# Kernel optimization log

Measured on AMD Instinct MI355X. Metric: run time of the kernel, lower is better.

Reference implementation:

```python
import jax, jax.numpy as jnp
import numpy as np
from jax import lax

B, TENC, TMEL = 32, 512, 400
E, H, A, P, M, F, K = 512, 512, 512, 256, 128, 32, 31


def setup_inputs() -> dict:
    key = jax.random.key(0)
    ks = jax.random.split(key, 20)
    def rn(i, shape, fan_in):
        return jax.random.normal(ks[i], shape, jnp.float32) / np.float32(np.sqrt(fan_in))
    return dict(
        enc_outputs=jax.random.normal(ks[0], (B, TENC, 2 * E), jnp.float32),
        mel_spec_true=jax.random.normal(ks[1], (B, TMEL, M), jnp.float32),
        text_lens=jax.random.randint(ks[2], (B,), 0, TENC),
        mel_spec_lens=jax.random.randint(ks[3], (B,), 0, TMEL),
        max_text_len=TENC,
        pre_w1=rn(4, (M, P), M), pre_w2=rn(5, (P, P), P),
        attn_wi=rn(6, (P + E, 3 * H), P + E), attn_wh=rn(7, (H, 3 * H), H),
        attn_bi=jnp.zeros((3 * H,), jnp.float32), attn_bh=jnp.zeros((3 * H,), jnp.float32),
        q_w=rn(8, (H, A), H), k_w=rn(9, (2 * E, A), 2 * E),
        score_w=rn(10, (A, 1), A), score_b=jnp.zeros((1,), jnp.float32),
        loc_conv_w=rn(11, (F, 2, K), 2 * K), loc_w=rn(12, (F, A), F), loc_b=jnp.zeros((A,), jnp.float32),
        out_wi=rn(13, (A + H, 3 * H), A + H), out_wh=rn(14, (H, 3 * H), H),
        out_bi=jnp.zeros((3 * H,), jnp.float32), out_bh=jnp.zeros((3 * H,), jnp.float32),
        dec_w=rn(15, (H + A, M), H + A), dec_b=jnp.zeros((M,), jnp.float32),
        gate_w=rn(16, (H + A, 1), H + A), gate_b=jnp.zeros((1,), jnp.float32),
    )


def _gru_step(x, h, wi, wh, bi, bh):
    # single-step torch nn.GRU cell; gate order r, z, n
    gi = x @ wi + bi
    gh = h @ wh + bh
    ir, iz, inn = jnp.split(gi, 3, axis=-1)
    hr, hz, hn = jnp.split(gh, 3, axis=-1)
    r = jax.nn.sigmoid(ir + hr)
    z = jax.nn.sigmoid(iz + hz)
    n = jnp.tanh(inn + r * hn)
    return (1.0 - z) * n + z * h


def reference(enc_outputs, mel_spec_true, text_lens, mel_spec_lens, max_text_len,
              pre_w1, pre_w2, attn_wi, attn_wh, attn_bi, attn_bh,
              q_w, k_w, score_w, score_b, loc_conv_w, loc_w, loc_b,
              out_wi, out_wh, out_bi, out_bh, dec_w, dec_b, gate_w, gate_b):
    Bsz, Tenc, _ = enc_outputs.shape
    Tmel = mel_spec_true.shape[1]
    Hd = attn_wh.shape[0]
    Ad = k_w.shape[1]
    pad = (loc_conv_w.shape[2] - 1) // 2

    keys_p = enc_outputs @ k_w                                # [B,Tenc,A]
    enc_mask = jnp.arange(Tenc)[None, :] > text_lens[:, None]  # True = masked (t > len)

    def prenet(x):  # dropout disabled for determinism
        return jax.nn.relu(jax.nn.relu(x @ pre_w1) @ pre_w2)

    dec_in0 = prenet(jnp.zeros((Bsz, mel_spec_true.shape[2]), enc_outputs.dtype))
    carry0 = (jnp.zeros((Bsz, Hd), jnp.float32), jnp.zeros((Bsz, Hd), jnp.float32),
              jnp.zeros((Bsz, Tenc), jnp.float32), jnp.zeros((Bsz, Tenc), jnp.float32),
              jnp.zeros((Bsz, Ad), jnp.float32), dec_in0)

    def step(carry, _):
        h_attn, h_out, att_w, att_cum, ctx, dec_in = carry
        h_attn = _gru_step(jnp.concatenate([dec_in, ctx], -1), h_attn, attn_wi, attn_wh, attn_bi, attn_bh)
        loc_in = jnp.stack([att_w, att_cum], axis=1)           # [B,2,Tenc]
        loc = lax.conv_general_dilated(loc_in, loc_conv_w, (1,), [(pad, pad)],
                                       dimension_numbers=('NCH', 'OIH', 'NCH'))  # [B,F,Tenc]
        loc = jnp.swapaxes(loc, 1, 2) @ loc_w + loc_b          # [B,Tenc,A]
        q = (h_attn @ q_w)[:, None, :]                         # [B,1,A]
        s = (jnp.tanh(q + keys_p + loc) @ score_w + score_b)[..., 0]  # [B,Tenc]
        s = jnp.where(enc_mask, -jnp.inf, s)
        att_w = jax.nn.softmax(s, axis=1)
        ctx = jnp.einsum('bt,bta->ba', att_w, keys_p)
        att_cum = att_cum + att_w
        h_out = _gru_step(jnp.concatenate([h_attn, ctx], -1), h_out, out_wi, out_wh, out_bi, out_bh)
        att_h = jnp.concatenate([h_out, ctx], -1)
        mel = att_h @ dec_w + dec_b                            # [B,M]
        stop = (att_h @ gate_w + gate_b)[:, 0]                 # [B]
        dec_in = prenet(mel)                                   # teacher_force_ratio = 0
        return (h_attn, h_out, att_w, att_cum, ctx, dec_in), (mel, stop, att_w)

    _, (mels, gates, attns) = lax.scan(step, carry0, None, length=Tmel)
    mels = jnp.swapaxes(mels, 0, 1)    # [B,Tmel,M]
    gates = jnp.swapaxes(gates, 0, 1)  # [B,Tmel]
    attns = jnp.swapaxes(attns, 0, 1)  # [B,Tmel,Tenc]
    mel_mask = jnp.arange(Tmel)[None, :] > mel_spec_lens[:, None]
    masked_mel = jnp.where(mel_mask[:, :, None], 0.0, mels)
    masked_gate = jnp.where(mel_mask, 1000.0, gates)
    return masked_mel, masked_gate, attns, mel_mask
```

## Files before the change

### kernel.cpp

```cpp
#include <hip/hip_runtime.h>
#include <hip/hip_fp16.h>
#include <math.h>

#define NBLK 256
#define NTHR 1024

__device__ __forceinline__ float fast_rcp(float x) {
#if __has_builtin(__builtin_amdgcn_rcpf)
  return __builtin_amdgcn_rcpf(x);
#else
  return 1.f / x;
#endif
}
__device__ __forceinline__ float fast_sigmoid(float x) { return fast_rcp(1.f + __expf(-x)); }
__device__ __forceinline__ float fast_tanh(float x) { return 1.f - 2.f * fast_rcp(1.f + __expf(2.f * x)); }

union HU2 { unsigned int u; __half2 h; };
union HU4 { uint4 u; __half2 h[4]; };
__device__ __forceinline__ float2 cvt2(unsigned int u) { HU2 t; t.u = u; return __half22float2(t.h); }

__device__ __forceinline__ void sta(float* p, float v) {
  __hip_atomic_store(p, v, __ATOMIC_RELAXED, __HIP_MEMORY_SCOPE_AGENT);
}
__device__ __forceinline__ float lda(const float* p) {
  return __hip_atomic_load(p, __ATOMIC_RELAXED, __HIP_MEMORY_SCOPE_AGENT);
}
__device__ __forceinline__ int ldai(const int* p) {
  return __hip_atomic_load(p, __ATOMIC_RELAXED, __HIP_MEMORY_SCOPE_AGENT);
}
__device__ __forceinline__ void ntst(float* p, float v) { __builtin_nontemporal_store(v, p); }

struct Params {
  const float *enc, *pre_w1, *pre_w2, *attn_bi, *attn_bh;
  const float *q_w, *k_w, *score_w, *score_b, *conv_w, *loc_w, *loc_b;
  const float *out_bi, *out_bh, *dec_b, *gate_b;
  const float *attn_wi, *attn_wh, *out_wi, *out_wh, *dec_w, *gate_w;
  const int *text_lens, *mel_lens;
  __half *hkeys, *gw1T, *gw2T, *decT, *pre1T, *pre2T, *gateh, *locwh, *qwT;
  float *hA, *hO, *attw, *attcum, *decin, *ebuf, *zpart, *ctxacc, *ctxacc2, *stateZ;
  float *qbuf;
  int *done, *zdone, *done2, *hAdone, *qdone;
  float *out_mel, *out_gate, *out_attn, *out_mask;
};

__global__ __launch_bounds__(512) void k_keys(Params p) {
  __shared__ float sA[16][132];
  __shared__ float sB[16][68];
  int tid = threadIdx.x;
  int row0 = blockIdx.x * 128, col0 = blockIdx.y * 64;
  float acc[4][4] = {};
  int r = tid >> 2, kq = tid & 3;
  int tx = tid & 15, ty = tid >> 4;
  for (int k0 = 0; k0 < 1024; k0 += 16) {
    __syncthreads();
    float4 a4 = *(const float4*)(p.enc + (size_t)(row0 + r) * 1024 + k0 + kq * 4);
    sA[kq * 4 + 0][r] = a4.x; sA[kq * 4 + 1][r] = a4.y;
    sA[kq * 4 + 2][r] = a4.z; sA[kq * 4 + 3][r] = a4.w;
    if (tid < 256) {
      int kb = tid >> 4, nb = (tid & 15) * 4;
      float4 b4 = *(const float4*)(p.k_w + (size_t)(k0 + kb) * 512 + col0 + nb);
      sB[kb][nb + 0] = b4.x; sB[kb][nb + 1] = b4.y;
      sB[kb][nb + 2] = b4.z; sB[kb][nb + 3] = b4.w;
    }
    __syncthreads();
#pragma unroll
    for (int k = 0; k < 16; k++) {
      float ar[4], br[4];
#pragma unroll
      for (int i = 0; i < 4; i++) { ar[i] = sA[k][ty * 4 + i]; br[i] = sB[k][tx * 4 + i]; }
#pragma unroll
      for (int i = 0; i < 4; i++)
#pragma unroll
        for (int j = 0; j < 4; j++) acc[i][j] = fmaf(ar[i], br[j], acc[i][j]);
    }
  }
#pragma unroll
  for (int i = 0; i < 4; i++)
#pragma unroll
    for (int j = 0; j < 4; j++)
      p.hkeys[(size_t)(row0 + ty * 4 + i) * 512 + col0 + tx * 4 + j] = __float2half(acc[i][j]);
}

__global__ __launch_bounds__(256) void k_repack(Params p) {
  const int gsz = gridDim.x * 256;
  const int t0 = blockIdx.x * 256 + threadIdx.x;
  for (int i = t0; i < 1280 * 512; i += gsz) {
    int r = i >> 9, u = i & 511;
    const float* src = (r < 768) ? p.attn_wi + (size_t)r * 1536 : p.attn_wh + (size_t)(r - 768) * 1536;
    __half2* d = (__half2*)(p.gw1T + ((size_t)i << 2));
    d[0] = __halves2half2(__float2half(src[u]), __float2half(src[512 + u]));
    d[1] = __halves2half2(__float2half(src[1024 + u]), __float2half(0.f));
  }
  for (int i = t0; i < 1536 * 512; i += gsz) {
    int r = i >> 9, u = i & 511;
    const float* src = (r < 1024) ? p.out_wi + (size_t)r * 1536 : p.out_wh + (size_t)(r - 1024) * 1536;
    __half2* d = (__half2*)(p.gw2T + ((size_t)i << 2));
    d[0] = __halves2half2(__float2half(src[u]), __float2half(src[512 + u]));
    d[1] = __halves2half2(__float2half(src[1024 + u]), __float2half(0.f));
  }
  for (int i = t0; i < 512 * 512; i += gsz) {
    int k = i >> 9, a = i & 511;
    p.qwT[(size_t)a * 512 + k] = __float2half(p.q_w[(size_t)k * 512 + a]);
  }
  for (int i = t0; i < 1024 * 128; i += gsz) {
    int k = i >> 7, m = i & 127;
    p.decT[(size_t)m * 1024 + k] = __float2half(p.dec_w[(size_t)k * 128 + m]);
  }
  for (int i = t0; i < 1024; i += gsz) p.gateh[i] = __float2half(p.gate_w[i]);
  for (int i = t0; i < 16384; i += gsz) p.locwh[i] = __float2half(p.loc_w[i]);
  for (int i = t0; i < 128 * 256; i += gsz) {
    int m = i >> 8, pc = i & 255;
    p.pre1T[(size_t)pc * 128 + m] = __float2half(p.pre_w1[(size_t)m * 256 + pc]);
  }
  for (int i = t0; i < 256 * 256; i += gsz) {
    int k = i >> 8, pc = i & 255;
    p.pre2T[(size_t)pc * 256 + k] = __float2half(p.pre_w2[(size_t)k * 256 + pc]);
  }
  for (int i = t0; i < 106496; i += gsz) p.stateZ[i] = 0.f;
  for (int i = t0; i < 16384; i += gsz) p.ctxacc[i] = 0.f;
  for (int i = t0; i < 16384; i += gsz) p.ctxacc2[i] = 0.f;
  for (int i = t0; i < 2048; i += gsz) p.hAdone[i] = 0;
  for (int i = t0; i < 12800; i += gsz) {
    int b = i / 400, t = i - b * 400;
    p.out_mask[i] = (t > p.mel_lens[b]) ? 1.f : 0.f;
  }
}

struct SMemMega {
  __half keysL[64 * 512];
  float ctxL[4][520];
  float hA2[4][520];
  float hO2[4][520];
  float invZ[4];
  union {
    struct { float x[4][264]; float4 part4[16][64]; } gr;
    struct { float locS[64][33]; float aw[94]; float ac[94]; float hA_s[512];
             float qS[512]; float qp2[16][64]; float cpred[8][512]; float eS[64]; } s3;
    struct { float xh[1024]; float red[1024]; float mel[128]; float p1[256]; } s6;
  } u;
};

__device__ __forceinline__ void gchunk(const uint2* __restrict__ w,
                                       const float* __restrict__ x, int ks,
                                       int j0, int j1,
                                       float& a0, float& a1, float& a2) {
#pragma unroll 8
  for (int j = j0; j < j1; ++j) {
    uint2 wv = w[(size_t)j << 13];
    float xv = x[ks + (j << 4)];
    float2 f0 = cvt2(wv.x);
    float nf = cvt2(wv.y).x;
    a0 = fmaf(xv, f0.x, a0);
    a1 = fmaf(xv, f0.y, a1);
    a2 = fmaf(xv, nf, a2);
  }
}

__global__ __launch_bounds__(NTHR) void mega(Params p) {
  __shared__ SMemMega sm;
  const int blk = blockIdx.x, tid = threadIdx.x;
  const int ug = blk & 31, bg = blk >> 5, b0 = bg * 4;
  const int bS = blk & 31, t8 = blk >> 5, t0g = t8 << 6;
  const int bgS = bS >> 2;

  const int u_ = tid & 15, b2_ = (tid >> 4) & 3, ks_ = tid >> 6;
  const int uG_ = (ug << 4) + u_;
  const uint2* w1 = (const uint2*)p.gw1T + ((size_t)ks_ << 9) + uG_;
  const uint2* w2 = (const uint2*)p.gw2T + ((size_t)ks_ << 9) + uG_;

  {
    const uint4* src = (const uint4*)(p.hkeys + (((size_t)(bS << 9) + t0g) << 9));
    uint4* dst = (uint4*)sm.keysL;
    for (int i = tid; i < 4096; i += NTHR) dst[i] = src[i];
    for (int i = tid; i < 2048; i += NTHR) {
      sm.ctxL[i >> 9][i & 511] = 0.f;
      sm.hA2[i >> 9][i & 511] = 0.f;
      sm.hO2[i >> 9][i & 511] = 0.f;
    }
  }
  __syncthreads();

  float g1r = 0.f, g1z = 0.f, g1ni = 0.f, g1nh = 0.f;

#pragma clang loop unroll(disable)
  for (int step = 0; step < 400; step++) {
    const int par = step & 1;
    float* hA_prev = p.hA + par * 16384;
    float* hA_next = p.hA + (par ^ 1) * 16384;
    float* hO_prev = p.hO + par * 16384;
    float* hO_next = p.hO + (par ^ 1) * 16384;
    float* cCur = par ? p.ctxacc2 : p.ctxacc;
    float* cNxt = par ? p.ctxacc : p.ctxacc2;

    float r2 = 0.f, z2 = 0.f, ni2 = 0.f, nh2 = 0.f;

    {
      if (step > 0) {
        if (tid == 0) {
          while (ldai(&p.done2[bg * 16]) < 16 * step)
            __builtin_amdgcn_s_sleep(2);
        }
        __syncthreads();
      }
      for (int i = tid; i < 1024; i += NTHR)
        sm.u.gr.x[i >> 8][i & 255] = lda(&p.decin[((b0 + (i >> 8)) << 8) + (i & 255)]);
      for (int i = tid; i < 2048; i += NTHR)
        sm.hO2[i >> 9][i & 511] = lda(&hO_prev[((b0 + (i >> 9)) << 9) + (i & 511)]);
      __syncthreads();
      gchunk(w1, &sm.u.gr.x[b2_][0], ks_, 0, 16, g1r, g1z, g1ni);
      sm.u.gr.part4[ks_][(u_ << 2) + b2_] = make_float4(g1r, g1z, g1ni, g1nh);
      __syncthreads();
      if (tid < 64) {
        int uu = tid >> 2, bb2 = tid & 3;
        float4 s = make_float4(0.f, 0.f, 0.f, 0.f);
#pragma unroll
        for (int l = 0; l < 16; l++) {
          float4 v = sm.u.gr.part4[l][(uu << 2) + bb2];
          s.x += v.x; s.y += v.y; s.z += v.z; s.w += v.w;
        }
        int uGf = (ug << 4) + uu;
        float r = fast_sigmoid(s.x + p.attn_bi[uGf] + p.attn_bh[uGf]);
        float z = fast_sigmoid(s.y + p.attn_bi[512 + uGf] + p.attn_bh[512 + uGf]);
        float n = fast_tanh(s.z + p.attn_bi[1024 + uGf] + r * (s.w + p.attn_bh[1024 + uGf]));
        float hv = lda(&hA_prev[((b0 + bb2) << 9) + uGf]);
        sta(&hA_next[((b0 + bb2) << 9) + uGf], (1.f - z) * n + z * hv);
      }
      asm volatile("s_waitcnt vmcnt(0)" ::: "memory");
      if (tid == 0) atomicAdd(&p.hAdone[bg * 16], 1);
      gchunk(w2, &sm.hO2[b2_][0] - 1024, ks_, 64, 96, r2, z2, nh2);
    }

    {
      __syncthreads();
      for (int j = tid; j < 94; j += NTHR) {
        int pp = t0g - 15 + j;
        bool ok = (unsigned)pp < 512u;
        sm.u.s3.aw[j] = ok ? lda(&p.attw[(bS << 9) + pp]) : 0.f;
        sm.u.s3.ac[j] = ok ? lda(&p.attcum[(bS << 9) + pp]) : 0.f;
      }
      if (t8 == 0) {
        for (int i = tid; i < 512; i += NTHR) sta(&cNxt[(bS << 9) + i], 0.f);
      }
      __syncthreads();
      const int tlen = p.text_lens[bS];
      for (int i = tid; i < 2048; i += NTHR) {
        int tt = i >> 5, f = i & 31;
        const float* w0 = p.conv_w + f * 62;
        float a = 0.f;
#pragma unroll
        for (int k = 0; k < 31; k++)
          a = fmaf(w0[k], sm.u.s3.aw[tt + k], fmaf(w0[31 + k], sm.u.s3.ac[tt + k], a));
        sm.u.s3.locS[tt][f] = a;
      }
      if (tid == 0) {
        while (ldai(&p.hAdone[bgS * 16]) < 32 * (step + 1))
          __builtin_amdgcn_s_sleep(2);
      }
      __syncthreads();
      if (tid < 512) sm.u.s3.hA_s[tid] = lda(&hA_next[(bS << 9) + tid]);
      __syncthreads();
      {
        int a = tid & 63, ks = tid >> 6;
        const HU4* qp = (const HU4*)(p.qwT + (size_t)(t0g + a) * 512 + ks * 32);
        float q0 = 0.f, q1 = 0.f;
#pragma unroll
        for (int it = 0; it < 4; it++) {
          HU4 raw = qp[it];
          int kb = ks * 32 + it * 8;
#pragma unroll
          for (int h2 = 0; h2 < 4; h2++) {
            float2 w = __half22float2(raw.h[h2]);
            q0 = fmaf(sm.u.s3.hA_s[kb + h2 * 2], w.x, q0);
            q1 = fmaf(sm.u.s3.hA_s[kb + h2 * 2 + 1], w.y, q1);
          }
        }
        sm.u.s3.qp2[ks][a] = q0 + q1;
      }
      __syncthreads();
      if (tid < 64) {
        float s = 0.f;
#pragma unroll
        for (int l = 0; l < 16; l++) s += sm.u.s3.qp2[l][tid];
        sta(&p.qbuf[(bS << 9) + t0g + tid], s + p.loc_b[t0g + tid]);
      }
      if (tid == 0) {
        asm volatile("s_waitcnt vmcnt(0)" ::: "memory");
        atomicAdd(&p.qdone[bS * 16], 1);
      }
      const int lane = tid & 63, wv = tid >> 6;
      float acc[4][8] = {};
#pragma unroll 4
      for (int f = 0; f < 32; f++) {
        HU4 rw; rw.u = *(const uint4*)(p.locwh + (size_t)f * 512 + lane * 8);
        float2 w0 = __half22float2(rw.h[0]), w1 = __half22float2(rw.h[1]);
        float2 w2v = __half22float2(rw.h[2]), w3 = __half22float2(rw.h[3]);
#pragma unroll
        for (int j = 0; j < 4; j++) {
          float lf = sm.u.s3.locS[wv * 4 + j][f];
          acc[j][0] = fmaf(lf, w0.x, acc[j][0]); acc[j][1] = fmaf(lf, w0.y, acc[j][1]);
          acc[j][2] = fmaf(lf, w1.x, acc[j][2]); acc[j][3] = fmaf(lf, w1.y, acc[j][3]);
          acc[j][4] = fmaf(lf, w2v.x, acc[j][4]); acc[j][5] = fmaf(lf, w2v.y, acc[j][5]);
          acc[j][6] = fmaf(lf, w3.x, acc[j][6]); acc[j][7] = fmaf(lf, w3.y, acc[j][7]);
        }
      }
      if (tid == 0) {
        while (ldai(&p.qdone[bS * 16]) < 8 * (step + 1))
          __builtin_amdgcn_s_sleep(2);
      }
      __syncthreads();
      if (tid < 512) sm.u.s3.qS[tid] = lda(&p.qbuf[(bS << 9) + tid]);
      __syncthreads();
      float4 qA = *(const float4*)&sm.u.s3.qS[lane * 8];
      float4 qB = *(const float4*)&sm.u.s3.qS[lane * 8 + 4];
#pragma unroll
      for (int j = 0; j < 4; j++) {
        int tL = wv * 4 + j;
        HU4 raw; raw.u = *(const uint4*)&sm.keysL[tL * 512 + lane * 8];
        float2 k0 = __half22float2(raw.h[0]), k1 = __half22float2(raw.h[1]);
        float2 k2 = __half22float2(raw.h[2]), k3 = __half22float2(raw.h[3]);
        acc[j][0] += qA.x + k0.x; acc[j][1] += qA.y + k0.y;
        acc[j][2] += qA.z + k1.x; acc[j][3] += qA.w + k1.y;
        acc[j][4] += qB.x + k2.x; acc[j][5] += qB.y + k2.y;
        acc[j][6] += qB.z + k3.x; acc[j][7] += qB.w + k3.y;
      }
      float4 sA = *(const float4*)(p.score_w + lane * 8);
      float4 sB = *(const float4*)(p.score_w + lane * 8 + 4);
      float sbias = p.score_b[0];
      float e_reg[4];
#pragma unroll
      for (int j = 0; j < 4; j++) {
        float pv = fast_tanh(acc[j][0]) * sA.x + fast_tanh(acc[j][1]) * sA.y +
                   fast_tanh(acc[j][2]) * sA.z + fast_tanh(acc[j][3]) * sA.w +
                   fast_tanh(acc[j][4]) * sB.x + fast_tanh(acc[j][5]) * sB.y +
                   fast_tanh(acc[j][6]) * sB.z + fast_tanh(acc[j][7]) * sB.w;
#pragma unroll
        for (int off = 32; off > 0; off >>= 1) pv += __shfl_xor(pv, off, 64);
        int t = t0g + wv * 4 + j;
        e_reg[j] = (t > tlen) ? 0.f : __expf(pv + sbias);
      }
      if (lane == 0) {
#pragma unroll
        for (int j = 0; j < 4; j++) sm.u.s3.eS[wv * 4 + j] = e_reg[j];
      }
      float cp[8] = {0.f, 0.f, 0.f, 0.f, 0.f, 0.f, 0.f, 0.f};
#pragma unroll
      for (int j = 0; j < 4; j++) {
        int tL = wv * 4 + j;
        HU4 raw; raw.u = *(const uint4*)&sm.keysL[tL * 512 + lane * 8];
        float2 k0 = __half22float2(raw.h[0]), k1 = __half22float2(raw.h[1]);
        float2 k2 = __half22float2(raw.h[2]), k3 = __half22float2(raw.h[3]);
        float e = e_reg[j];
        cp[0] = fmaf(e, k0.x, cp[0]); cp[1] = fmaf(e, k0.y, cp[1]);
        cp[2] = fmaf(e, k1.x, cp[2]); cp[3] = fmaf(e, k1.y, cp[3]);
        cp[4] = fmaf(e, k2.x, cp[4]); cp[5] = fmaf(e, k2.y, cp[5]);
        cp[6] = fmaf(e, k3.x, cp[6]); cp[7] = fmaf(e, k3.y, cp[7]);
      }
      __syncthreads();
      if (wv < 8) {
        float4* r0 = (float4*)&sm.u.s3.cpred[wv][lane * 8];
        r0[0] = make_float4(cp[0], cp[1], cp[2], cp[3]);
        r0[1] = make_float4(cp[4], cp[5], cp[6], cp[7]);
      }
      __syncthreads();
      if (wv >= 8) {
        float* r0 = &sm.u.s3.cpred[wv - 8][lane * 8];
#pragma unroll
        for (int i = 0; i < 8; i++) r0[i] += cp[i];
      }
      __syncthreads();
      if (tid < 512) {
        float s = 0.f;
#pragma unroll
        for (int j = 0; j < 8; j++) s += sm.u.s3.cpred[j][tid];
        atomicAdd(&cCur[(bS << 9) + tid], s);
      }
      if (tid < 64) {
        float e = sm.u.s3.eS[tid];
        sta(&p.ebuf[(bS << 9) + t0g + tid], e);
        float z = e;
#pragma unroll
        for (int off = 32; off > 0; off >>= 1) z += __shfl_xor(z, off, 64);
        if (tid == 0) sta(&p.zpart[bS * 8 + t8], z);
      }
      if (tid < 512 && (tid & 63) == 0) {
        asm volatile("s_waitcnt vmcnt(0)" ::: "memory");
        atomicAdd(&p.zdone[bgS * 16], 1);
      }
      if (tid == 0) {
        while (ldai(&p.hAdone[bg * 16]) < 32 * (step + 1))
          __builtin_amdgcn_s_sleep(2);
      }
      __syncthreads();
      for (int i = tid; i < 2048; i += NTHR)
        sm.hA2[i >> 9][i & 511] = lda(&hA_next[((b0 + (i >> 9)) << 9) + (i & 511)]);
      __syncthreads();
      gchunk(w2, &sm.hA2[b2_][0], ks_, 0, 32, r2, z2, ni2);
    }

    {
      if (tid == 0) {
        while (ldai(&p.zdone[bg * 16]) < 256 * (step + 1))
          __builtin_amdgcn_s_sleep(2);
      }
      __syncthreads();
      if (tid < 4) {
        float Z = 0.f;
#pragma unroll
        for (int j = 0; j < 8; j++) Z += lda(&p.zpart[(b0 + tid) * 8 + j]);
        sm.invZ[tid] = fast_rcp(Z);
      }
      __syncthreads();
      for (int i = tid; i < 2048; i += NTHR) {
        int b2 = i >> 9, a = i & 511;
        sm.ctxL[b2][a] = lda(&cCur[((b0 + b2) << 9) + a]) * sm.invZ[b2];
      }
      if (ug < 4 && tid < 512) {
        const int bb = b0 + ug;
        float v = lda(&p.ebuf[(bb << 9) + tid]) * sm.invZ[ug];
        sta(&p.attw[(bb << 9) + tid], v);
        float oc = lda(&p.attcum[(bb << 9) + tid]);
        sta(&p.attcum[(bb << 9) + tid], oc + v);
        ntst(&p.out_attn[(size_t)bb * 204800 + (size_t)step * 512 + tid], v);
      }
      __syncthreads();
      gchunk(w2, &sm.ctxL[b2_][0] - 512, ks_, 32, 64, r2, z2, ni2);
      sm.u.gr.part4[ks_][(u_ << 2) + b2_] = make_float4(r2, z2, ni2, nh2);
      __syncthreads();
      if (tid < 64) {
        int uu = tid >> 2, bb2 = tid & 3;
        float4 s = make_float4(0.f, 0.f, 0.f, 0.f);
#pragma unroll
        for (int l = 0; l < 16; l++) {
          float4 v = sm.u.gr.part4[l][(uu << 2) + bb2];
          s.x += v.x; s.y += v.y; s.z += v.z; s.w += v.w;
        }
        int uGf = (ug << 4) + uu;
        float r = fast_sigmoid(s.x + p.out_bi[uGf] + p.out_bh[uGf]);
        float z = fast_sigmoid(s.y + p.out_bi[512 + uGf] + p.out_bh[512 + uGf]);
        float n = fast_tanh(s.z + p.out_bi[1024 + uGf] + r * (s.w + p.out_bh[1024 + uGf]));
        float hv = sm.hO2[bb2][uGf];
        sta(&hO_next[((b0 + bb2) << 9) + uGf], (1.f - z) * n + z * hv);
      }
      asm volatile("s_waitcnt vmcnt(0)" ::: "memory");
      if (tid == 0) atomicAdd(&p.done[bg * 16], 1);
      g1r = 0.f; g1z = 0.f; g1ni = 0.f; g1nh = 0.f;
      if (step < 399) {
        gchunk(w1, &sm.ctxL[b2_][0] - 256, ks_, 16, 48, g1r, g1z, g1ni);
        gchunk(w1, &sm.hA2[b2_][0] - 768, ks_, 48, 80, g1r, g1z, g1nh);
      }
      if (ug < 4) {
        const int bb = b0 + ug;
        if (tid == 0) {
          while (ldai(&p.done[bg * 16]) < 32 * (step + 1))
            __builtin_amdgcn_s_sleep(2);
        }
        __syncthreads();
        sm.u.s6.xh[tid] = (tid < 512) ? lda(&hO_next[(bb << 9) + tid])
                                      : sm.ctxL[ug][tid - 512];
        __syncthreads();
        bool masked = step > p.mel_lens[bb];
        {
          int m = tid & 127, ks = tid >> 7;
          const HU4* dp = (const HU4*)(p.decT + (size_t)m * 1024 + ks * 128);
          float a = 0.f;
#pragma unroll 4
          for (int it = 0; it < 16; it++) {
            HU4 raw = dp[it];
            int kb = ks * 128 + it * 8;
#pragma unroll
            for (int h2 = 0; h2 < 4; h2++) {
              float2 w = __half22float2(raw.h[h2]);
              a = fmaf(sm.u.s6.xh[kb + h2 * 2], w.x, a);
              a = fmaf(sm.u.s6.xh[kb + h2 * 2 + 1], w.y, a);
            }
          }
          sm.u.s6.red[tid] = a;
        }
        __syncthreads();
        if (tid < 128) {
          float mv = p.dec_b[tid];
#pragma unroll
          for (int j = 0; j < 8; j++) mv += sm.u.s6.red[tid + j * 128];
          sm.u.s6.mel[tid] = mv;
          ntst(&p.out_mel[(size_t)bb * 51200 + (size_t)step * 128 + tid], masked ? 0.f : mv);
        }
        __syncthreads();
        sm.u.s6.red[tid] = sm.u.s6.xh[tid] * __half2float(p.gateh[tid]);
        __syncthreads();
        if (tid < 64) {
          float g = 0.f;
#pragma unroll
          for (int j = 0; j < 16; j++) g += sm.u.s6.red[tid + j * 64];
#pragma unroll
          for (int off = 32; off > 0; off >>= 1) g += __shfl_xor(g, off, 64);
          if (tid == 0) ntst(&p.out_gate[bb * 400 + step], masked ? 1000.f : (g + p.gate_b[0]));
        }
        __syncthreads();
        {
          int pc = tid & 255, ks = tid >> 8;
          const HU4* wp = (const HU4*)(p.pre1T + (size_t)pc * 128 + ks * 32);
          float a = 0.f;
#pragma unroll
          for (int it = 0; it < 4; it++) {
            HU4 raw = wp[it];
            int kb = ks * 32 + it * 8;
#pragma unroll
            for (int h2 = 0; h2 < 4; h2++) {
              float2 w = __half22float2(raw.h[h2]);
              a = fmaf(sm.u.s6.mel[kb + h2 * 2], w.x, a);
              a = fmaf(sm.u.s6.mel[kb + h2 * 2 + 1], w.y, a);
            }
          }
          sm.u.s6.red[tid] = a;
        }
        __syncthreads();
        if (tid < 256) {
          float a = sm.u.s6.red[tid] + sm.u.s6.red[tid + 256] +
                    sm.u.s6.red[tid + 512] + sm.u.s6.red[tid + 768];
          sm.u.s6.p1[tid] = fmaxf(a, 0.f);
        }
        __syncthreads();
        {
          int pc = tid & 255, ks = tid >> 8;
          const HU4* wp = (const HU4*)(p.pre2T + (size_t)pc * 256 + ks * 64);
          float a = 0.f;
#pragma unroll
          for (int it = 0; it < 8; it++) {
            HU4 raw = wp[it];
            int kb = ks * 64 + it * 8;
#pragma unroll
            for (int h2 = 0; h2 < 4; h2++) {
              float2 w = __half22float2(raw.h[h2]);
              a = fmaf(sm.u.s6.p1[kb + h2 * 2], w.x, a);
              a = fmaf(sm.u.s6.p1[kb + h2 * 2 + 1], w.y, a);
            }
          }
          sm.u.s6.red[tid] = a;
        }
        __syncthreads();
        if (tid < 256) {
          float a = sm.u.s6.red[tid] + sm.u.s6.red[tid + 256] +
                    sm.u.s6.red[tid + 512] + sm.u.s6.red[tid + 768];
          sta(&p.decin[(bb << 8) + tid], fmaxf(a, 0.f));
        }
        if (tid < 256 && (tid & 63) == 0) {
          asm volatile("s_waitcnt vmcnt(0)" ::: "memory");
          atomicAdd(&p.done2[bg * 16], 1);
        }
      }
    }
  }
}

extern "C" void kernel_launch(void* const* d_in, const int* in_sizes, int n_in,
                              void* d_out, int out_size, void* d_ws, size_t ws_size,
                              hipStream_t stream) {
  Params p;
  p.enc       = (const float*)d_in[0];
  p.text_lens = (const int*)d_in[2];
  p.mel_lens  = (const int*)d_in[3];
  p.pre_w1    = (const float*)d_in[5];
  p.pre_w2    = (const float*)d_in[6];
  p.attn_wi   = (const float*)d_in[7];
  p.attn_wh   = (const float*)d_in[8];
  p.attn_bi   = (const float*)d_in[9];
  p.attn_bh   = (const float*)d_in[10];
  p.q_w       = (const float*)d_in[11];
  p.k_w       = (const float*)d_in[12];
  p.score_w   = (const float*)d_in[13];
  p.score_b   = (const float*)d_in[14];
  p.conv_w    = (const float*)d_in[15];
  p.loc_w     = (const float*)d_in[16];
  p.loc_b     = (const float*)d_in[17];
  p.out_wi    = (const float*)d_in[18];
  p.out_wh    = (const float*)d_in[19];
  p.out_bi    = (const float*)d_in[20];
  p.out_bh    = (const float*)d_in[21];
  p.dec_w     = (const float*)d_in[22];
  p.dec_b     = (const float*)d_in[23];
  p.gate_w    = (const float*)d_in[24];
  p.gate_b    = (const float*)d_in[25];

  float* ws = (float*)d_ws;
  p.hkeys  = (__half*)(ws);
  p.gw1T   = (__half*)(ws + 4194304);
  p.gw2T   = (__half*)(ws + 5505024);
  p.decT   = (__half*)(ws + 7077888);
  p.pre1T  = (__half*)(ws + 7143424);
  p.pre2T  = (__half*)(ws + 7159808);
  p.gateh  = (__half*)(ws + 7192576);
  p.locwh  = (__half*)(ws + 7193088);
  p.qwT    = (__half*)(ws + 7201280);
  p.hA     = ws + 7332352;
  p.hO     = ws + 7365120;
  p.attw   = ws + 7397888;
  p.attcum = ws + 7414272;
  p.decin  = ws + 7430656;
  p.stateZ = p.hA;
  p.ebuf   = ws + 7438848;
  p.zpart  = ws + 7455232;
  p.ctxacc = ws + 7455488;
  p.ctxacc2 = ws + 7472416;
  int* fb  = (int*)(ws + 7488800);
  p.hAdone = fb;
  p.zdone  = fb + 128;
  p.done   = fb + 256;
  p.done2  = fb + 384;
  p.qdone  = fb + 512;
  p.qbuf   = ws + 7490848;
  float* out = (float*)d_out;
  p.out_mel  = out;
  p.out_gate = out + 1638400;
  p.out_attn = out + 1651200;
  p.out_mask = out + 8204800;

  k_repack<<<2048, 256, 0, stream>>>(p);
  k_keys<<<dim3(128, 8), 512, 0, stream>>>(p);
  void* args[] = { (void*)&p };
  hipLaunchCooperativeKernel((const void*)mega, dim3(NBLK), dim3(NTHR), args, 0, stream);
}
```

Before: 37.33 ms.

## Distribute mel/gate projection across GRU blocks via partial sums and offload attention writes

Each block that computes a 16-unit slice of the output GRU state now also computes partial dot products of its hO/ctx slice with dec_w and gate_w (read as fp32). These partials go to a global buffer, which the owning block sums over 32 slices. The per-batch block no longer does the full 1024x128 decoder matvec on the serial critical path. The attention-weight normalisation and stores move from the ug<4 blocks to ug 4..7, so that work runs in parallel. Other changes come with this: a one-time global barrier (melpart reuses the hkeys workspace region), higher done counters, and extra synchronisation and global traffic for the partials.

```diff
diff --git a/kernel.cpp b/kernel.cpp
--- a/kernel.cpp
+++ b/kernel.cpp
@@ -36,10 +36,10 @@
   const float *out_bi, *out_bh, *dec_b, *gate_b;
   const float *attn_wi, *attn_wh, *out_wi, *out_wh, *dec_w, *gate_w;
   const int *text_lens, *mel_lens;
-  __half *hkeys, *gw1T, *gw2T, *decT, *pre1T, *pre2T, *gateh, *locwh, *qwT;
+  __half *hkeys, *gw1T, *gw2T, *pre1T, *pre2T, *locwh, *qwT;
   float *hA, *hO, *attw, *attcum, *decin, *ebuf, *zpart, *ctxacc, *ctxacc2, *stateZ;
-  float *qbuf;
-  int *done, *zdone, *done2, *hAdone, *qdone;
+  float *qbuf, *melpart, *gatepart;
+  int *done, *zdone, *done2, *hAdone, *qdone, *initbar;
   float *out_mel, *out_gate, *out_attn, *out_mask;
 };
 
@@ -102,11 +102,6 @@
     int k = i >> 9, a = i & 511;
     p.qwT[(size_t)a * 512 + k] = __float2half(p.q_w[(size_t)k * 512 + a]);
   }
-  for (int i = t0; i < 1024 * 128; i += gsz) {
-    int k = i >> 7, m = i & 127;
-    p.decT[(size_t)m * 1024 + k] = __float2half(p.dec_w[(size_t)k * 128 + m]);
-  }
-  for (int i = t0; i < 1024; i += gsz) p.gateh[i] = __float2half(p.gate_w[i]);
   for (int i = t0; i < 16384; i += gsz) p.locwh[i] = __float2half(p.loc_w[i]);
   for (int i = t0; i < 128 * 256; i += gsz) {
     int m = i >> 8, pc = i & 255;
@@ -133,10 +128,10 @@
   float hO2[4][520];
   float invZ[4];
   union {
-    struct { float x[4][264]; float4 part4[16][64]; } gr;
+    struct { float x[4][264]; float4 part4[16][64]; float hOslice[4][16]; } gr;
     struct { float locS[64][33]; float aw[94]; float ac[94]; float hA_s[512];
              float qS[512]; float qp2[16][64]; float cpred[8][512]; float eS[64]; } s3;
-    struct { float xh[1024]; float red[1024]; float mel[128]; float p1[256]; } s6;
+    struct { float red[1024]; float mel[132]; float p1[264]; } s6;
   } u;
 };
 
@@ -179,6 +174,11 @@
     }
   }
   __syncthreads();
+  if (tid == 0) {
+    atomicAdd(p.initbar, 1);
+    while (ldai(p.initbar) < NBLK) __builtin_amdgcn_s_sleep(2);
+  }
+  __syncthreads();
 
   float g1r = 0.f, g1z = 0.f, g1ni = 0.f, g1nh = 0.f;
 
@@ -197,7 +197,7 @@
     {
       if (step > 0) {
         if (tid == 0) {
-          while (ldai(&p.done2[bg * 16]) < 16 * step)
+          while (ldai(&p.done2[bg * 16]) < 48 * step)
             __builtin_amdgcn_s_sleep(2);
         }
         __syncthreads();
@@ -414,14 +414,6 @@
         int b2 = i >> 9, a = i & 511;
         sm.ctxL[b2][a] = lda(&cCur[((b0 + b2) << 9) + a]) * sm.invZ[b2];
       }
-      if (ug < 4 && tid < 512) {
-        const int bb = b0 + ug;
-        float v = lda(&p.ebuf[(bb << 9) + tid]) * sm.invZ[ug];
-        sta(&p.attw[(bb << 9) + tid], v);
-        float oc = lda(&p.attcum[(bb << 9) + tid]);
-        sta(&p.attcum[(bb << 9) + tid], oc + v);
-        ntst(&p.out_attn[(size_t)bb * 204800 + (size_t)step * 512 + tid], v);
-      }
       __syncthreads();
       gchunk(w2, &sm.ctxL[b2_][0] - 512, ks_, 32, 64, r2, z2, ni2);
       sm.u.gr.part4[ks_][(u_ << 2) + b2_] = make_float4(r2, z2, ni2, nh2);
@@ -439,10 +431,37 @@
         float z = fast_sigmoid(s.y + p.out_bi[512 + uGf] + p.out_bh[512 + uGf]);
         float n = fast_tanh(s.z + p.out_bi[1024 + uGf] + r * (s.w + p.out_bh[1024 + uGf]));
         float hv = sm.hO2[bb2][uGf];
-        sta(&hO_next[((b0 + bb2) << 9) + uGf], (1.f - z) * n + z * hv);
-      }
-      asm volatile("s_waitcnt vmcnt(0)" ::: "memory");
-      if (tid == 0) atomicAdd(&p.done[bg * 16], 1);
+        float hnew = (1.f - z) * n + z * hv;
+        sta(&hO_next[((b0 + bb2) << 9) + uGf], hnew);
+        sm.u.gr.hOslice[bb2][uu] = hnew;
+      }
+      __syncthreads();
+      if (tid < 512) {
+        int b = tid >> 7, m = tid & 127;
+        const float* dwH = p.dec_w + ((size_t)(ug << 4)) * 128 + m;
+        const float* dwC = p.dec_w + ((size_t)(512 + (ug << 4))) * 128 + m;
+        float a = 0.f;
+#pragma unroll
+        for (int u = 0; u < 16; u++) {
+          a = fmaf(sm.u.gr.hOslice[b][u], dwH[(size_t)u * 128], a);
+          a = fmaf(sm.ctxL[b][(ug << 4) + u], dwC[(size_t)u * 128], a);
+        }
+        sta(&p.melpart[((((b0 + b) << 5) | ug) << 7) + m], a);
+        if (m == 0) {
+          const float* gw = p.gate_w + (ug << 4);
+          float g = 0.f;
+#pragma unroll
+          for (int u = 0; u < 16; u++) {
+            g = fmaf(sm.u.gr.hOslice[b][u], gw[u], g);
+            g = fmaf(sm.ctxL[b][(ug << 4) + u], gw[512 + u], g);
+          }
+          sta(&p.gatepart[((b0 + b) << 5) | ug], g);
+        }
+      }
+      if (tid < 512 && (tid & 63) == 0) {
+        asm volatile("s_waitcnt vmcnt(0)" ::: "memory");
+        atomicAdd(&p.done[bg * 16], 1);
+      }
       g1r = 0.f; g1z = 0.f; g1ni = 0.f; g1nh = 0.f;
       if (step < 399) {
         gchunk(w1, &sm.ctxL[b2_][0] - 256, ks_, 16, 48, g1r, g1z, g1ni);
@@ -451,49 +470,26 @@
       if (ug < 4) {
         const int bb = b0 + ug;
         if (tid == 0) {
-          while (ldai(&p.done[bg * 16]) < 32 * (step + 1))
+          while (ldai(&p.done[bg * 16]) < 256 * (step + 1))
             __builtin_amdgcn_s_sleep(2);
         }
-        __syncthreads();
-        sm.u.s6.xh[tid] = (tid < 512) ? lda(&hO_next[(bb << 9) + tid])
-                                      : sm.ctxL[ug][tid - 512];
         __syncthreads();
         bool masked = step > p.mel_lens[bb];
-        {
-          int m = tid & 127, ks = tid >> 7;
-          const HU4* dp = (const HU4*)(p.decT + (size_t)m * 1024 + ks * 128);
-          float a = 0.f;
-#pragma unroll 4
-          for (int it = 0; it < 16; it++) {
-            HU4 raw = dp[it];
-            int kb = ks * 128 + it * 8;
-#pragma unroll
-            for (int h2 = 0; h2 < 4; h2++) {
-              float2 w = __half22float2(raw.h[h2]);
-              a = fmaf(sm.u.s6.xh[kb + h2 * 2], w.x, a);
-              a = fmaf(sm.u.s6.xh[kb + h2 * 2 + 1], w.y, a);
-            }
-          }
-          sm.u.s6.red[tid] = a;
-        }
-        __syncthreads();
         if (tid < 128) {
+          const float* mp = p.melpart + (((size_t)(bb << 5)) << 7) + tid;
           float mv = p.dec_b[tid];
 #pragma unroll
-          for (int j = 0; j < 8; j++) mv += sm.u.s6.red[tid + j * 128];
+          for (int g = 0; g < 32; g++) mv += lda(mp + (g << 7));
           sm.u.s6.mel[tid] = mv;
           ntst(&p.out_mel[(size_t)bb * 51200 + (size_t)step * 128 + tid], masked ? 0.f : mv);
         }
-        __syncthreads();
-        sm.u.s6.red[tid] = sm.u.s6.xh[tid] * __half2float(p.gateh[tid]);
-        __syncthreads();
-        if (tid < 64) {
-          float g = 0.f;
-#pragma unroll
-          for (int j = 0; j < 16; j++) g += sm.u.s6.red[tid + j * 64];
-#pragma unroll
-          for (int off = 32; off > 0; off >>= 1) g += __shfl_xor(g, off, 64);
-          if (tid == 0) ntst(&p.out_gate[bb * 400 + step], masked ? 1000.f : (g + p.gate_b[0]));
+        if (tid >= 128 && tid < 192) {
+          int l = tid & 63;
+          float g = (l < 32) ? lda(&p.gatepart[(bb << 5) + l]) : 0.f;
+#pragma unroll
+          for (int off = 16; off > 0; off >>= 1) g += __shfl_xor(g, off, 64);
+          if (l == 0)
+            ntst(&p.out_gate[bb * 400 + step], masked ? 1000.f : (g + p.gate_b[0]));
         }
         __syncthreads();
         {
@@ -544,6 +540,19 @@
           sta(&p.decin[(bb << 8) + tid], fmaxf(a, 0.f));
         }
         if (tid < 256 && (tid & 63) == 0) {
+          asm volatile("s_waitcnt vmcnt(0)" ::: "memory");
+          atomicAdd(&p.done2[bg * 16], 1);
+        }
+      } else if (ug < 8) {
+        const int bj = ug - 4, bb = b0 + bj;
+        if (tid < 512) {
+          float v = lda(&p.ebuf[(bb << 9) + tid]) * sm.invZ[bj];
+          sta(&p.attw[(bb << 9) + tid], v);
+          float oc = lda(&p.attcum[(bb << 9) + tid]);
+          sta(&p.attcum[(bb << 9) + tid], oc + v);
+          ntst(&p.out_attn[(size_t)bb * 204800 + (size_t)step * 512 + tid], v);
+        }
+        if (tid < 512 && (tid & 63) == 0) {
           asm volatile("s_waitcnt vmcnt(0)" ::: "memory");
           atomicAdd(&p.done2[bg * 16], 1);
         }
@@ -583,12 +592,12 @@
 
   float* ws = (float*)d_ws;
   p.hkeys  = (__half*)(ws);
+  p.melpart = ws;
+  p.gatepart = ws + 131072;
   p.gw1T   = (__half*)(ws + 4194304);
   p.gw2T   = (__half*)(ws + 5505024);
-  p.decT   = (__half*)(ws + 7077888);
   p.pre1T  = (__half*)(ws + 7143424);
   p.pre2T  = (__half*)(ws + 7159808);
-  p.gateh  = (__half*)(ws + 7192576);
   p.locwh  = (__half*)(ws + 7193088);
   p.qwT    = (__half*)(ws + 7201280);
   p.hA     = ws + 7332352;
@@ -607,6 +616,7 @@
   p.done   = fb + 256;
   p.done2  = fb + 384;
   p.qdone  = fb + 512;
+  p.initbar = fb + 1920;
   p.qbuf   = ws + 7490848;
   float* out = (float*)d_out;
   p.out_mel  = out;
```

New measurement: 46.05 ms. 1.23x slower.

## Replicate decoder/prenet per block to remove the done2 grid barrier

Applied to the files above, without the earlier changes.

Every block in a batch group now recomputes the mel projection and both prenet layers for its 4 batch rows redundantly, keeping decoder input in shared memory instead of waiting on a done2 flag from 4 designated blocks. hA and hO previous values are also read from local shared copies. The attention-weight normalisation and attcum update move to different blocks after the GRU, with a new per-batch adone counter that the attention stage waits on. This swaps a cross-block dependency on the serial critical path for redundant matmul work in every block, and risks ordering or visibility problems in the new flag protocol.

```diff
diff --git a/kernel.cpp b/kernel.cpp
--- a/kernel.cpp
+++ b/kernel.cpp
@@ -39,7 +39,7 @@
   __half *hkeys, *gw1T, *gw2T, *decT, *pre1T, *pre2T, *gateh, *locwh, *qwT;
   float *hA, *hO, *attw, *attcum, *decin, *ebuf, *zpart, *ctxacc, *ctxacc2, *stateZ;
   float *qbuf;
-  int *done, *zdone, *done2, *hAdone, *qdone;
+  int *done, *zdone, *hAdone, *qdone, *adone;
   float *out_mel, *out_gate, *out_attn, *out_mask;
 };
 
@@ -131,12 +131,13 @@
   float ctxL[4][520];
   float hA2[4][520];
   float hO2[4][520];
+  float decinL[4][264];
   float invZ[4];
   union {
-    struct { float x[4][264]; float4 part4[16][64]; } gr;
+    struct { float pad[1056]; float4 part4[16][64]; } gr;
     struct { float locS[64][33]; float aw[94]; float ac[94]; float hA_s[512];
              float qS[512]; float qp2[16][64]; float cpred[8][512]; float eS[64]; } s3;
-    struct { float xh[1024]; float red[1024]; float mel[128]; float p1[256]; } s6;
+    struct { float red[4][264]; float mel[4][132]; float p1[4][264]; } s6;
   } u;
 };
 
@@ -177,6 +178,7 @@
       sm.hA2[i >> 9][i & 511] = 0.f;
       sm.hO2[i >> 9][i & 511] = 0.f;
     }
+    for (int i = tid; i < 1024; i += NTHR) sm.decinL[i >> 8][i & 255] = 0.f;
   }
   __syncthreads();
 
@@ -185,9 +187,7 @@
 #pragma clang loop unroll(disable)
   for (int step = 0; step < 400; step++) {
     const int par = step & 1;
-    float* hA_prev = p.hA + par * 16384;
     float* hA_next = p.hA + (par ^ 1) * 16384;
-    float* hO_prev = p.hO + par * 16384;
     float* hO_next = p.hO + (par ^ 1) * 16384;
     float* cCur = par ? p.ctxacc2 : p.ctxacc;
     float* cNxt = par ? p.ctxacc : p.ctxacc2;
@@ -195,19 +195,7 @@
     float r2 = 0.f, z2 = 0.f, ni2 = 0.f, nh2 = 0.f;
 
     {
-      if (step > 0) {
-        if (tid == 0) {
-          while (ldai(&p.done2[bg * 16]) < 16 * step)
-            __builtin_amdgcn_s_sleep(2);
-        }
-        __syncthreads();
-      }
-      for (int i = tid; i < 1024; i += NTHR)
-        sm.u.gr.x[i >> 8][i & 255] = lda(&p.decin[((b0 + (i >> 8)) << 8) + (i & 255)]);
-      for (int i = tid; i < 2048; i += NTHR)
-        sm.hO2[i >> 9][i & 511] = lda(&hO_prev[((b0 + (i >> 9)) << 9) + (i & 511)]);
-      __syncthreads();
-      gchunk(w1, &sm.u.gr.x[b2_][0], ks_, 0, 16, g1r, g1z, g1ni);
+      gchunk(w1, &sm.decinL[b2_][0], ks_, 0, 16, g1r, g1z, g1ni);
       sm.u.gr.part4[ks_][(u_ << 2) + b2_] = make_float4(g1r, g1z, g1ni, g1nh);
       __syncthreads();
       if (tid < 64) {
@@ -222,7 +210,7 @@
         float r = fast_sigmoid(s.x + p.attn_bi[uGf] + p.attn_bh[uGf]);
         float z = fast_sigmoid(s.y + p.attn_bi[512 + uGf] + p.attn_bh[512 + uGf]);
         float n = fast_tanh(s.z + p.attn_bi[1024 + uGf] + r * (s.w + p.attn_bh[1024 + uGf]));
-        float hv = lda(&hA_prev[((b0 + bb2) << 9) + uGf]);
+        float hv = sm.hA2[bb2][uGf];
         sta(&hA_next[((b0 + bb2) << 9) + uGf], (1.f - z) * n + z * hv);
       }
       asm volatile("s_waitcnt vmcnt(0)" ::: "memory");
@@ -232,6 +220,13 @@
 
     {
       __syncthreads();
+      if (step > 0) {
+        if (tid == 0) {
+          while (ldai(&p.adone[bS * 16]) < 8 * step)
+            __builtin_amdgcn_s_sleep(2);
+        }
+        __syncthreads();
+      }
       for (int j = tid; j < 94; j += NTHR) {
         int pp = t0g - 15 + j;
         bool ok = (unsigned)pp < 512u;
@@ -414,14 +409,6 @@
         int b2 = i >> 9, a = i & 511;
         sm.ctxL[b2][a] = lda(&cCur[((b0 + b2) << 9) + a]) * sm.invZ[b2];
       }
-      if (ug < 4 && tid < 512) {
-        const int bb = b0 + ug;
-        float v = lda(&p.ebuf[(bb << 9) + tid]) * sm.invZ[ug];
-        sta(&p.attw[(bb << 9) + tid], v);
-        float oc = lda(&p.attcum[(bb << 9) + tid]);
-        sta(&p.attcum[(bb << 9) + tid], oc + v);
-        ntst(&p.out_attn[(size_t)bb * 204800 + (size_t)step * 512 + tid], v);
-      }
       __syncthreads();
       gchunk(w2, &sm.ctxL[b2_][0] - 512, ks_, 32, 64, r2, z2, ni2);
       sm.u.gr.part4[ks_][(u_ << 2) + b2_] = make_float4(r2, z2, ni2, nh2);
@@ -443,111 +430,132 @@
       }
       asm volatile("s_waitcnt vmcnt(0)" ::: "memory");
       if (tid == 0) atomicAdd(&p.done[bg * 16], 1);
+      if (ug >= 4 && ug < 8) {
+        const int bj = ug - 4, bb = b0 + bj;
+        if (tid < 512) {
+          float v = lda(&p.ebuf[(bb << 9) + tid]) * sm.invZ[bj];
+          sta(&p.attw[(bb << 9) + tid], v);
+          float oc = lda(&p.attcum[(bb << 9) + tid]);
+          sta(&p.attcum[(bb << 9) + tid], oc + v);
+          ntst(&p.out_attn[(size_t)bb * 204800 + (size_t)step * 512 + tid], v);
+        }
+        if (tid < 512 && (tid & 63) == 0) {
+          asm volatile("s_waitcnt vmcnt(0)" ::: "memory");
+          atomicAdd(&p.adone[bb * 16], 1);
+        }
+      }
       g1r = 0.f; g1z = 0.f; g1ni = 0.f; g1nh = 0.f;
       if (step < 399) {
         gchunk(w1, &sm.ctxL[b2_][0] - 256, ks_, 16, 48, g1r, g1z, g1ni);
         gchunk(w1, &sm.hA2[b2_][0] - 768, ks_, 48, 80, g1r, g1z, g1nh);
       }
-      if (ug < 4) {
-        const int bb = b0 + ug;
-        if (tid == 0) {
-          while (ldai(&p.done[bg * 16]) < 32 * (step + 1))
-            __builtin_amdgcn_s_sleep(2);
-        }
-        __syncthreads();
-        sm.u.s6.xh[tid] = (tid < 512) ? lda(&hO_next[(bb << 9) + tid])
-                                      : sm.ctxL[ug][tid - 512];
-        __syncthreads();
-        bool masked = step > p.mel_lens[bb];
-        {
-          int m = tid & 127, ks = tid >> 7;
-          const HU4* dp = (const HU4*)(p.decT + (size_t)m * 1024 + ks * 128);
-          float a = 0.f;
-#pragma unroll 4
-          for (int it = 0; it < 16; it++) {
-            HU4 raw = dp[it];
-            int kb = ks * 128 + it * 8;
-#pragma unroll
-            for (int h2 = 0; h2 < 4; h2++) {
-              float2 w = __half22float2(raw.h[h2]);
-              a = fmaf(sm.u.s6.xh[kb + h2 * 2], w.x, a);
-              a = fmaf(sm.u.s6.xh[kb + h2 * 2 + 1], w.y, a);
-            }
+      if (tid == 0) {
+        while (ldai(&p.done[bg * 16]) < 32 * (step + 1))
+          __builtin_amdgcn_s_sleep(2);
+      }
+      __syncthreads();
+      for (int i = tid; i < 2048; i += NTHR)
+        sm.hO2[i >> 9][i & 511] = lda(&hO_next[((b0 + (i >> 9)) << 9) + (i & 511)]);
+      __syncthreads();
+      if (tid < 256) {
+        int m = tid & 127, kh = tid >> 7;
+        const HU4* dp = (const HU4*)(p.decT + (size_t)m * 1024 + kh * 512);
+        const float* base = kh ? &sm.ctxL[0][0] : &sm.hO2[0][0];
+        float a0 = 0.f, a1 = 0.f, a2 = 0.f, a3 = 0.f;
+#pragma unroll 8
+        for (int it = 0; it < 64; it++) {
+          HU4 raw = dp[it];
+          int kb = it * 8;
+#pragma unroll
+          for (int h2 = 0; h2 < 4; h2++) {
+            float2 w = __half22float2(raw.h[h2]);
+            int k0 = kb + h2 * 2, k1 = k0 + 1;
+            a0 = fmaf(base[k0], w.x, fmaf(base[k1], w.y, a0));
+            a1 = fmaf(base[520 + k0], w.x, fmaf(base[520 + k1], w.y, a1));
+            a2 = fmaf(base[1040 + k0], w.x, fmaf(base[1040 + k1], w.y, a2));
+            a3 = fmaf(base[1560 + k0], w.x, fmaf(base[1560 + k1], w.y, a3));
           }
-          sm.u.s6.red[tid] = a;
-        }
-        __syncthreads();
-        if (tid < 128) {
-          float mv = p.dec_b[tid];
-#pragma unroll
-          for (int j = 0; j < 8; j++) mv += sm.u.s6.red[tid + j * 128];
-          sm.u.s6.mel[tid] = mv;
-          ntst(&p.out_mel[(size_t)bb * 51200 + (size_t)step * 128 + tid], masked ? 0.f : mv);
-        }
-        __syncthreads();
-        sm.u.s6.red[tid] = sm.u.s6.xh[tid] * __half2float(p.gateh[tid]);
-        __syncthreads();
-        if (tid < 64) {
-          float g = 0.f;
-#pragma unroll
-          for (int j = 0; j < 16; j++) g += sm.u.s6.red[tid + j * 64];
-#pragma unroll
-          for (int off = 32; off > 0; off >>= 1) g += __shfl_xor(g, off, 64);
-          if (tid == 0) ntst(&p.out_gate[bb * 400 + step], masked ? 1000.f : (g + p.gate_b[0]));
-        }
-        __syncthreads();
-        {
-          int pc = tid & 255, ks = tid >> 8;
-          const HU4* wp = (const HU4*)(p.pre1T + (size_t)pc * 128 + ks * 32);
-          float a = 0.f;
-#pragma unroll
-          for (int it = 0; it < 4; it++) {
-            HU4 raw = wp[it];
-            int kb = ks * 32 + it * 8;
-#pragma unroll
-            for (int h2 = 0; h2 < 4; h2++) {
-              float2 w = __half22float2(raw.h[h2]);
-              a = fmaf(sm.u.s6.mel[kb + h2 * 2], w.x, a);
-              a = fmaf(sm.u.s6.mel[kb + h2 * 2 + 1], w.y, a);
-            }
+        }
+        int idx = kh * 128 + m;
+        sm.u.s6.red[0][idx] = a0; sm.u.s6.red[1][idx] = a1;
+        sm.u.s6.red[2][idx] = a2; sm.u.s6.red[3][idx] = a3;
+      }
+      __syncthreads();
+      if (tid < 512) {
+        int b = tid >> 7, m = tid & 127;
+        float mv = p.dec_b[m] + sm.u.s6.red[b][m] + sm.u.s6.red[b][128 + m];
+        sm.u.s6.mel[b][m] = mv;
+        if (ug < 4 && b == ug) {
+          int bb = b0 + b;
+          bool masked = step > p.mel_lens[bb];
+          ntst(&p.out_mel[(size_t)bb * 51200 + (size_t)step * 128 + m], masked ? 0.f : mv);
+        }
+      }
+      __syncthreads();
+      if (ug < 4 && tid >= 512 && tid < 768) {
+        int t = tid - 512;
+        float g = sm.hO2[ug][t] * __half2float(p.gateh[t]) +
+                  sm.hO2[ug][t + 256] * __half2float(p.gateh[t + 256]) +
+                  sm.ctxL[ug][t] * __half2float(p.gateh[512 + t]) +
+                  sm.ctxL[ug][t + 256] * __half2float(p.gateh[768 + t]);
+        sm.u.s6.red[0][t] = g;
+      }
+      if (tid < 256) {
+        int pc = tid;
+        const HU4* wp = (const HU4*)(p.pre1T + (size_t)pc * 128);
+        float a0 = 0.f, a1 = 0.f, a2 = 0.f, a3 = 0.f;
+#pragma unroll
+        for (int it = 0; it < 16; it++) {
+          HU4 raw = wp[it];
+          int kb = it * 8;
+#pragma unroll
+          for (int h2 = 0; h2 < 4; h2++) {
+            float2 w = __half22float2(raw.h[h2]);
+            int k0 = kb + h2 * 2, k1 = k0 + 1;
+            a0 = fmaf(sm.u.s6.mel[0][k0], w.x, fmaf(sm.u.s6.mel[0][k1], w.y, a0));
+            a1 = fmaf(sm.u.s6.mel[1][k0], w.x, fmaf(sm.u.s6.mel[1][k1], w.y, a1));
+            a2 = fmaf(sm.u.s6.mel[2][k0], w.x, fmaf(sm.u.s6.mel[2][k1], w.y, a2));
+            a3 = fmaf(sm.u.s6.mel[3][k0], w.x, fmaf(sm.u.s6.mel[3][k1], w.y, a3));
           }
-          sm.u.s6.red[tid] = a;
-        }
-        __syncthreads();
-        if (tid < 256) {
-          float a = sm.u.s6.red[tid] + sm.u.s6.red[tid + 256] +
-                    sm.u.s6.red[tid + 512] + sm.u.s6.red[tid + 768];
-          sm.u.s6.p1[tid] = fmaxf(a, 0.f);
-        }
-        __syncthreads();
-        {
-          int pc = tid & 255, ks = tid >> 8;
-          const HU4* wp = (const HU4*)(p.pre2T + (size_t)pc * 256 + ks * 64);
-          float a = 0.f;
-#pragma unroll
-          for (int it = 0; it < 8; it++) {
-            HU4 raw = wp[it];
-            int kb = ks * 64 + it * 8;
-#pragma unroll
-            for (int h2 = 0; h2 < 4; h2++) {
-              float2 w = __half22float2(raw.h[h2]);
-              a = fmaf(sm.u.s6.p1[kb + h2 * 2], w.x, a);
-              a = fmaf(sm.u.s6.p1[kb + h2 * 2 + 1], w.y, a);
-            }
+        }
+        sm.u.s6.p1[0][pc] = fmaxf(a0, 0.f); sm.u.s6.p1[1][pc] = fmaxf(a1, 0.f);
+        sm.u.s6.p1[2][pc] = fmaxf(a2, 0.f); sm.u.s6.p1[3][pc] = fmaxf(a3, 0.f);
+      }
+      __syncthreads();
+      if (ug < 4 && tid >= 512 && tid < 576) {
+        int l = tid - 512;
+        float g = sm.u.s6.red[0][l] + sm.u.s6.red[0][l + 64] +
+                  sm.u.s6.red[0][l + 128] + sm.u.s6.red[0][l + 192];
+#pragma unroll
+        for (int off = 32; off > 0; off >>= 1) g += __shfl_xor(g, off, 64);
+        if (l == 0) {
+          int bb = b0 + ug;
+          bool masked = step > p.mel_lens[bb];
+          ntst(&p.out_gate[bb * 400 + step], masked ? 1000.f : (g + p.gate_b[0]));
+        }
+      }
+      if (tid < 256) {
+        int pc = tid;
+        const HU4* wp = (const HU4*)(p.pre2T + (size_t)pc * 256);
+        float a0 = 0.f, a1 = 0.f, a2 = 0.f, a3 = 0.f;
+#pragma unroll 8
+        for (int it = 0; it < 32; it++) {
+          HU4 raw = wp[it];
+          int kb = it * 8;
+#pragma unroll
+          for (int h2 = 0; h2 < 4; h2++) {
+            float2 w = __half22float2(raw.h[h2]);
+            int k0 = kb + h2 * 2, k1 = k0 + 1;
+            a0 = fmaf(sm.u.s6.p1[0][k0], w.x, fmaf(sm.u.s6.p1[0][k1], w.y, a0));
+            a1 = fmaf(sm.u.s6.p1[1][k0], w.x, fmaf(sm.u.s6.p1[1][k1], w.y, a1));
+            a2 = fmaf(sm.u.s6.p1[2][k0], w.x, fmaf(sm.u.s6.p1[2][k1], w.y, a2));
+            a3 = fmaf(sm.u.s6.p1[3][k0], w.x, fmaf(sm.u.s6.p1[3][k1], w.y, a3));
           }
-          sm.u.s6.red[tid] = a;
-        }
-        __syncthreads();
-        if (tid < 256) {
-          float a = sm.u.s6.red[tid] + sm.u.s6.red[tid + 256] +
-                    sm.u.s6.red[tid + 512] + sm.u.s6.red[tid + 768];
-          sta(&p.decin[(bb << 8) + tid], fmaxf(a, 0.f));
-        }
-        if (tid < 256 && (tid & 63) == 0) {
-          asm volatile("s_waitcnt vmcnt(0)" ::: "memory");
-          atomicAdd(&p.done2[bg * 16], 1);
-        }
-      }
+        }
+        sm.decinL[0][pc] = fmaxf(a0, 0.f); sm.decinL[1][pc] = fmaxf(a1, 0.f);
+        sm.decinL[2][pc] = fmaxf(a2, 0.f); sm.decinL[3][pc] = fmaxf(a3, 0.f);
+      }
+      __syncthreads();
     }
   }
 }
@@ -605,8 +613,8 @@
   p.hAdone = fb;
   p.zdone  = fb + 128;
   p.done   = fb + 256;
-  p.done2  = fb + 384;
   p.qdone  = fb + 512;
+  p.adone  = fb + 1024;
   p.qbuf   = ws + 7490848;
   float* out = (float*)d_out;
   p.out_mel  = out;
```

Measured after the change: 42.08 ms. +12.7%, slower.
